# Kernel tuning notes

Measured on AMD Instinct MI355X. Metric: run time of the kernel, lower is better.

## Reference

```python
import jax, jax.numpy as jnp
import numpy as np

TOP_K = 4
EPS = 1e-6


def setup_inputs() -> dict:
    key = jax.random.key(0)
    k1, k2, k3 = jax.random.split(key, 3)
    B, Q, N, H, W = 4, 200, 32, 256, 256
    pred_masks = jax.random.normal(k1, (B, Q, H, W), dtype=jnp.float32)
    pred_logits = jax.random.normal(k2, (B, Q, 2), dtype=jnp.float32)
    gt_masks = (jax.random.uniform(k3, (B, N, H, W)) < 0.3).astype(jnp.float32)
    return {"pred_masks": pred_masks, "pred_logits": pred_logits, "gt_masks": gt_masks}


def _combined_scores(pred_masks, pred_logits, gt_masks):
    """IoU * class-score, shape [B, Q, N]."""
    pm = jax.nn.sigmoid(pred_masks)                    # [B,Q,H,W]
    cls = jax.nn.softmax(pred_logits, axis=-1)[..., 1]  # [B,Q]
    B, Q = pm.shape[:2]
    N = gt_masks.shape[1]
    pmf = pm.reshape(B, Q, -1)                         # [B,Q,D]
    tmf = gt_masks.reshape(B, N, -1)                   # [B,N,D]
    inter = jnp.einsum('bqd,bnd->bqn', pmf, tmf)
    union = pmf.sum(-1)[:, :, None] + tmf.sum(-1)[:, None, :] - inter
    iou = inter / (union + EPS)
    return iou * cls[:, :, None]


def _greedy_assign(combined):
    """Greedy per-GT top-k with dedup. combined: [Q,N] -> sel indices [N,k], -1 = dropped."""
    Q = combined.shape[0]
    k = min(TOP_K, Q)

    def step(assigned, col):
        _, idx = jax.lax.top_k(col, k)          # [k] query indices for this GT
        taken = assigned[idx]                   # already assigned -> drop
        sel = jnp.where(taken, -1, idx)
        assigned = assigned.at[idx].set(True)
        return assigned, sel

    _, sels = jax.lax.scan(step, jnp.zeros(Q, dtype=bool), combined.T)
    return sels  # [N, k]


def reference(pred_masks, pred_logits, gt_masks):
    combined = _combined_scores(pred_masks, pred_logits, gt_masks)  # [B,Q,N]
    sels = jax.vmap(_greedy_assign)(combined)                       # [B,N,k]
    B, N, k = sels.shape
    src_idx = sels
    tgt_idx = jnp.broadcast_to(jnp.arange(N, dtype=jnp.int32)[None, :, None], sels.shape)
    valid = sels >= 0
    tgt_idx = jnp.where(valid, tgt_idx, -1)
    return src_idx, tgt_idx, valid
```

## Files before the change

kernel.cpp:

```cpp
#include <hip/hip_runtime.h>
#include <math.h>
#include <stdint.h>

#define BB    4
#define QQ    200
#define NGT   32
#define DD    65536
#define TOPK  4
#define EPSF  1e-6f
#define QP    208

#define QT3   7
#define KG    64
#define NSTEP 16

typedef float  f32x4  __attribute__((ext_vector_type(4)));
typedef float  f32x16 __attribute__((ext_vector_type(16)));
typedef __bf16 bf16x8 __attribute__((ext_vector_type(8)));

__global__ __launch_bounds__(256) void k_pack(const float* __restrict__ gt,
                                              uint32_t* __restrict__ packed,
                                              float* __restrict__ zero_base) {
    int zidx = blockIdx.x * 256 + threadIdx.x;
    if (zidx < BB * NGT * QP + BB * QP) zero_base[zidx] = 0.0f;

    int blk = blockIdx.x;
    int b = blk >> 6;
    int d0 = ((blk & 63) * 256 + threadIdx.x) * 4;
    uint32_t px = 0, py = 0, pz = 0, pw = 0;
    const float* gb = gt + (size_t)b * NGT * DD + d0;
#pragma unroll
    for (int n = 0; n < NGT; ++n) {
        float4 g = *(const float4*)(gb + (size_t)n * DD);
        px |= (g.x > 0.5f ? 1u : 0u) << n;
        py |= (g.y > 0.5f ? 1u : 0u) << n;
        pz |= (g.z > 0.5f ? 1u : 0u) << n;
        pw |= (g.w > 0.5f ? 1u : 0u) << n;
    }
    *(uint4*)(packed + (size_t)b * DD + d0) = make_uint4(px, py, pz, pw);
}

__global__ __launch_bounds__(256) void k_tsum(const uint32_t* __restrict__ packed,
                                              float* __restrict__ tsum) {
    int b = blockIdx.x >> 5;
    int n = blockIdx.x & 31;
    const uint4* pp = (const uint4*)(packed + (size_t)b * DD);
    int cnt = 0;
    for (int i = threadIdx.x; i < DD / 4; i += 256) {
        uint4 w = pp[i];
        cnt += (int)((w.x >> n) & 1u) + (int)((w.y >> n) & 1u) +
               (int)((w.z >> n) & 1u) + (int)((w.w >> n) & 1u);
    }
#pragma unroll
    for (int off = 32; off; off >>= 1) cnt += __shfl_xor(cnt, off);
    __shared__ int red[4];
    if ((threadIdx.x & 63) == 0) red[threadIdx.x >> 6] = cnt;
    __syncthreads();
    if (threadIdx.x == 0)
        tsum[blockIdx.x] = (float)(red[0] + red[1] + red[2] + red[3]);
}

__global__ __launch_bounds__(256, 4) void k_mfma(const float* __restrict__ pm,
                                                 const uint32_t* __restrict__ packed,
                                                 float* __restrict__ inter,
                                                 float* __restrict__ psum) {
    int blk = blockIdx.x;
    int b   = blk / (QT3 * KG);
    int rem = blk % (QT3 * KG);
    int qt  = rem / KG;
    int kg  = rem % KG;
    int tid = threadIdx.x, lane = tid & 63, wave = tid >> 6;
    int m = lane & 31, half = lane >> 5;

    int q_glob = qt * 32 + m;
    int q_eff  = q_glob < QQ ? q_glob : QQ - 1;
    int kbase  = kg * 1024 + wave * 256;
    const float*    ap = pm + (size_t)(b * QQ + q_eff) * DD + kbase + half * 8;
    const uint32_t* bp = packed + (size_t)b * DD + kbase + half * 8;

    f32x16 c0, c1;
#pragma unroll
    for (int r = 0; r < 16; ++r) { c0[r] = 0.f; c1[r] = 0.f; }
    float ps = 0.f;
    int sh = 31 - m;

    float4 fa0 = *(const float4*)ap;
    float4 fa1 = *(const float4*)(ap + 4);
    uint4  wb0 = *(const uint4*)bp;
    uint4  wb1 = *(const uint4*)(bp + 4);

    for (int s = 0; s < NSTEP; ++s) {
        float4 a0 = fa0, a1 = fa1;
        uint4  w0 = wb0, w1 = wb1;
        if (s < NSTEP - 1) {
            const float*    apn = ap + (s + 1) * 16;
            const uint32_t* bpn = bp + (s + 1) * 16;
            fa0 = *(const float4*)apn;
            fa1 = *(const float4*)(apn + 4);
            wb0 = *(const uint4*)bpn;
            wb1 = *(const uint4*)(bpn + 4);
        }
        float xs[8] = {a0.x, a0.y, a0.z, a0.w, a1.x, a1.y, a1.z, a1.w};
        uint32_t hu[8], mu[8], lu[8];
#pragma unroll
        for (int i = 0; i < 8; ++i) {
            float x  = xs[i];
            float sg = __builtin_amdgcn_rcpf(1.0f + __expf(-x));
            ps += sg;
            uint32_t u0 = __float_as_uint(sg);
            float hi = __uint_as_float(u0 & 0xFFFF0000u);
            float r1 = sg - hi;
            uint32_t u1 = __float_as_uint(r1);
            float mi = __uint_as_float(u1 & 0xFFFF0000u);
            float r2 = r1 - mi;
            hu[i] = u0; mu[i] = u1; lu[i] = __float_as_uint(r2);
        }
        union { uint4 u; bf16x8 v; } ah, am, al, bb;
        ah.u = make_uint4((hu[0] >> 16) | (hu[1] & 0xFFFF0000u),
                          (hu[2] >> 16) | (hu[3] & 0xFFFF0000u),
                          (hu[4] >> 16) | (hu[5] & 0xFFFF0000u),
                          (hu[6] >> 16) | (hu[7] & 0xFFFF0000u));
        am.u = make_uint4((mu[0] >> 16) | (mu[1] & 0xFFFF0000u),
                          (mu[2] >> 16) | (mu[3] & 0xFFFF0000u),
                          (mu[4] >> 16) | (mu[5] & 0xFFFF0000u),
                          (mu[6] >> 16) | (mu[7] & 0xFFFF0000u));
        al.u = make_uint4((lu[0] >> 16) | (lu[1] & 0xFFFF0000u),
                          (lu[2] >> 16) | (lu[3] & 0xFFFF0000u),
                          (lu[4] >> 16) | (lu[5] & 0xFFFF0000u),
                          (lu[6] >> 16) | (lu[7] & 0xFFFF0000u));
        uint32_t wj[8] = {w0.x, w0.y, w0.z, w0.w, w1.x, w1.y, w1.z, w1.w};
        uint32_t bv[4];
#pragma unroll
        for (int d = 0; d < 4; ++d)
            bv[d] = ((uint32_t)(((int)(wj[2 * d] << sh)) >> 31) & 0x3F80u)
                  | ((uint32_t)(((int)(wj[2 * d + 1] << sh)) >> 31) & 0x3F800000u);
        bb.u = make_uint4(bv[0], bv[1], bv[2], bv[3]);

        c0 = __builtin_amdgcn_mfma_f32_32x32x16_bf16(ah.v, bb.v, c0, 0, 0, 0);
        c1 = __builtin_amdgcn_mfma_f32_32x32x16_bf16(am.v, bb.v, c1, 0, 0, 0);
        c1 = __builtin_amdgcn_mfma_f32_32x32x16_bf16(al.v, bb.v, c1, 0, 0, 0);
    }

    ps += __shfl_xor(ps, 32);
    if (lane < 32 && q_glob < QQ) atomicAdd(&psum[b * QP + q_glob], ps);

    f32x16 c;
#pragma unroll
    for (int r = 0; r < 16; ++r) c[r] = c0[r] + c1[r];

    __shared__ float cred[3 * 64 * 17];
    if (wave > 0) {
        float* dst = cred + ((wave - 1) * 64 + lane) * 17;
#pragma unroll
        for (int r = 0; r < 16; ++r) dst[r] = c[r];
    }
    __syncthreads();
    if (wave == 0) {
#pragma unroll
        for (int wv = 0; wv < 3; ++wv) {
            const float* sp = cred + (wv * 64 + lane) * 17;
#pragma unroll
            for (int r = 0; r < 16; ++r) c[r] += sp[r];
        }
#pragma unroll
        for (int r = 0; r < 16; ++r) {
            int qg = qt * 32 + (r & 3) + 8 * (r >> 2) + 4 * half;
            if (qg < QQ) atomicAdd(&inter[(b * NGT + m) * QP + qg], c[r]);
        }
    }
}

__global__ __launch_bounds__(64) void k_topk(const float* __restrict__ inter,
                                             const float* __restrict__ psum,
                                             const float* __restrict__ tsum,
                                             const float* __restrict__ logits,
                                             int* __restrict__ idx4) {
    int bn = blockIdx.x;
    int b  = bn >> 5;
    int lane = threadIdx.x;
    float tsn = tsum[bn];
    float v[4];
#pragma unroll
    for (int s = 0; s < 4; ++s) {
        int q = lane + 64 * s;
        if (q < QQ) {
            float iv = inter[(size_t)bn * QP + q];
            float un = psum[b * QP + q] + tsn - iv;
            float l0 = logits[(b * QQ + q) * 2];
            float l1 = logits[(b * QQ + q) * 2 + 1];
            float cl = 1.0f / (1.0f + expf(l0 - l1));
            v[s] = iv / (un + EPSF) * cl;
        } else {
            v[s] = -INFINITY;
        }
    }
    for (int k = 0; k < TOPK; ++k) {
        float bv = -INFINITY;
        int   bi = 0x7fffffff;
#pragma unroll
        for (int s = 0; s < 4; ++s)
            if (v[s] > bv) { bv = v[s]; bi = lane + 64 * s; }
#pragma unroll
        for (int off = 32; off; off >>= 1) {
            float ov = __shfl_xor(bv, off);
            int   oi = __shfl_xor(bi, off);
            if (ov > bv || (ov == bv && oi < bi)) { bv = ov; bi = oi; }
        }
        if (lane == (bi & 63)) v[bi >> 6] = -INFINITY;
        if (lane == 0) idx4[bn * TOPK + k] = bi;
    }
}

__global__ __launch_bounds__(64) void k_final(const int* __restrict__ idx4,
                                              int* __restrict__ out) {
    int b = blockIdx.x;
    int lane = threadIdx.x;
    int* src = out;
    int* tgt = out + BB * NGT * TOPK;
    int* val = out + 2 * BB * NGT * TOPK;
    int asg = 0;
    for (int n = 0; n < NGT; ++n) {
        int4 id = *(const int4*)&idx4[(b * NGT + n) * TOPK];
        int ids[4] = {id.x, id.y, id.z, id.w};
        int newasg = asg;
#pragma unroll
        for (int k = 0; k < TOPK; ++k) {
            int idx = ids[k];
            int owner = idx & 63, slot = idx >> 6;
            int oasg = __shfl(asg, owner);
            int taken = (oasg >> slot) & 1;
            if (lane == owner) newasg |= (1 << slot);
            if (lane == 0) {
                int o = (b * NGT + n) * TOPK + k;
                src[o] = taken ? -1 : idx;
                tgt[o] = taken ? -1 : n;
                val[o] = taken ? 0 : 1;
            }
        }
        asg = newasg;
    }
}

extern "C" void kernel_launch(void* const* d_in, const int* in_sizes, int n_in,
                              void* d_out, int out_size, void* d_ws, size_t ws_size,
                              hipStream_t stream) {
    const float* pred_masks  = (const float*)d_in[0];
    const float* pred_logits = (const float*)d_in[1];
    const float* gt_masks    = (const float*)d_in[2];

    uint8_t* ws = (uint8_t*)d_ws;
    uint32_t* packed = (uint32_t*)ws;
    float* tsum  = (float*)(ws + (size_t)BB * DD * 4);
    float* inter = tsum + BB * NGT;
    float* psum  = inter + BB * NGT * QP;
    int*   idx4  = (int*)(psum + BB * QP);

    k_pack <<<BB * (DD / 1024), 256, 0, stream>>>(gt_masks, packed, inter);
    k_tsum <<<BB * NGT,         256, 0, stream>>>(packed, tsum);
    k_mfma <<<BB * QT3 * KG,    256, 0, stream>>>(pred_masks, packed, inter, psum);
    k_topk <<<BB * NGT,          64, 0, stream>>>(inter, psum, tsum, pred_logits, idx4);
    k_final<<<BB,                64, 0, stream>>>(idx4, (int*)d_out);
}
```

Before: 382.9 us.

## Restructure MFMA kernel into 16x16x32 tiles with double-buffered LDS staging

```diff
diff --git a/kernel.cpp b/kernel.cpp
--- a/kernel.cpp
+++ b/kernel.cpp
@@ -10,13 +10,20 @@
 #define EPSF  1e-6f
 #define QP    208
 
-#define QT3   7
-#define KG    64
-#define NSTEP 16
+#define QT16  13
+#define KG    16
+#define KSPAN (DD / KG)
+#define BK    256
+#define NCH   (KSPAN / BK)
+#define RS    260
 
 typedef float  f32x4  __attribute__((ext_vector_type(4)));
-typedef float  f32x16 __attribute__((ext_vector_type(16)));
 typedef __bf16 bf16x8 __attribute__((ext_vector_type(8)));
+
+#define GLOAD_LDS16(gp, lp)                                                       \
+    __builtin_amdgcn_global_load_lds(                                             \
+        (const __attribute__((address_space(1))) void*)(gp),                      \
+        (__attribute__((address_space(3))) void*)(lp), 16, 0, 0)
 
 __global__ __launch_bounds__(256) void k_pack(const float* __restrict__ gt,
                                               uint32_t* __restrict__ packed,
@@ -65,107 +72,135 @@
                                                  float* __restrict__ inter,
                                                  float* __restrict__ psum) {
     int blk = blockIdx.x;
-    int b   = blk / (QT3 * KG);
-    int rem = blk % (QT3 * KG);
+    int b   = blk / (QT16 * KG);
+    int rem = blk % (QT16 * KG);
     int qt  = rem / KG;
     int kg  = rem % KG;
     int tid = threadIdx.x, lane = tid & 63, wave = tid >> 6;
-    int m = lane & 31, half = lane >> 5;
-
-    int q_glob = qt * 32 + m;
-    int q_eff  = q_glob < QQ ? q_glob : QQ - 1;
-    int kbase  = kg * 1024 + wave * 256;
-    const float*    ap = pm + (size_t)(b * QQ + q_eff) * DD + kbase + half * 8;
-    const uint32_t* bp = packed + (size_t)b * DD + kbase + half * 8;
-
-    f32x16 c0, c1;
-#pragma unroll
-    for (int r = 0; r < 16; ++r) { c0[r] = 0.f; c1[r] = 0.f; }
+    int m = lane & 15, quad = lane >> 4;
+
+    __shared__ float    sA[2][16][RS];
+    __shared__ uint32_t sB[2][BK];
+
+    const size_t kbase = (size_t)kg * KSPAN;
+    const float*    pmb = pm + (size_t)b * QQ * DD + kbase;
+    const uint32_t* pkb = packed + (size_t)b * DD + kbase;
+
+    auto stage = [&](int c, int bf) {
+#pragma unroll
+        for (int i = 0; i < 4; ++i) {
+            int row = wave * 4 + i;
+            int qg  = qt * 16 + row;
+            int qe  = qg < QQ ? qg : QQ - 1;
+            const float* gp = pmb + (size_t)qe * DD + c * BK + lane * 4;
+            GLOAD_LDS16(gp, &sA[bf][row][0]);
+        }
+        if (wave == 0) {
+            const uint32_t* gp = pkb + c * BK + lane * 4;
+            GLOAD_LDS16(gp, &sB[bf][0]);
+        }
+    };
+
+    f32x4 cH0 = {0.f,0.f,0.f,0.f}, cL0 = {0.f,0.f,0.f,0.f};
+    f32x4 cH1 = {0.f,0.f,0.f,0.f}, cL1 = {0.f,0.f,0.f,0.f};
     float ps = 0.f;
-    int sh = 31 - m;
-
-    float4 fa0 = *(const float4*)ap;
-    float4 fa1 = *(const float4*)(ap + 4);
-    uint4  wb0 = *(const uint4*)bp;
-    uint4  wb1 = *(const uint4*)(bp + 4);
-
-    for (int s = 0; s < NSTEP; ++s) {
-        float4 a0 = fa0, a1 = fa1;
-        uint4  w0 = wb0, w1 = wb1;
-        if (s < NSTEP - 1) {
-            const float*    apn = ap + (s + 1) * 16;
-            const uint32_t* bpn = bp + (s + 1) * 16;
-            fa0 = *(const float4*)apn;
-            fa1 = *(const float4*)(apn + 4);
-            wb0 = *(const uint4*)bpn;
-            wb1 = *(const uint4*)(bpn + 4);
-        }
-        float xs[8] = {a0.x, a0.y, a0.z, a0.w, a1.x, a1.y, a1.z, a1.w};
-        uint32_t hu[8], mu[8], lu[8];
-#pragma unroll
-        for (int i = 0; i < 8; ++i) {
-            float x  = xs[i];
-            float sg = __builtin_amdgcn_rcpf(1.0f + __expf(-x));
-            ps += sg;
-            uint32_t u0 = __float_as_uint(sg);
-            float hi = __uint_as_float(u0 & 0xFFFF0000u);
-            float r1 = sg - hi;
-            uint32_t u1 = __float_as_uint(r1);
-            float mi = __uint_as_float(u1 & 0xFFFF0000u);
-            float r2 = r1 - mi;
-            hu[i] = u0; mu[i] = u1; lu[i] = __float_as_uint(r2);
-        }
-        union { uint4 u; bf16x8 v; } ah, am, al, bb;
-        ah.u = make_uint4((hu[0] >> 16) | (hu[1] & 0xFFFF0000u),
-                          (hu[2] >> 16) | (hu[3] & 0xFFFF0000u),
-                          (hu[4] >> 16) | (hu[5] & 0xFFFF0000u),
-                          (hu[6] >> 16) | (hu[7] & 0xFFFF0000u));
-        am.u = make_uint4((mu[0] >> 16) | (mu[1] & 0xFFFF0000u),
-                          (mu[2] >> 16) | (mu[3] & 0xFFFF0000u),
-                          (mu[4] >> 16) | (mu[5] & 0xFFFF0000u),
-                          (mu[6] >> 16) | (mu[7] & 0xFFFF0000u));
-        al.u = make_uint4((lu[0] >> 16) | (lu[1] & 0xFFFF0000u),
-                          (lu[2] >> 16) | (lu[3] & 0xFFFF0000u),
-                          (lu[4] >> 16) | (lu[5] & 0xFFFF0000u),
-                          (lu[6] >> 16) | (lu[7] & 0xFFFF0000u));
-        uint32_t wj[8] = {w0.x, w0.y, w0.z, w0.w, w1.x, w1.y, w1.z, w1.w};
-        uint32_t bv[4];
-#pragma unroll
-        for (int d = 0; d < 4; ++d)
-            bv[d] = ((uint32_t)(((int)(wj[2 * d] << sh)) >> 31) & 0x3F80u)
-                  | ((uint32_t)(((int)(wj[2 * d + 1] << sh)) >> 31) & 0x3F800000u);
-        bb.u = make_uint4(bv[0], bv[1], bv[2], bv[3]);
-
-        c0 = __builtin_amdgcn_mfma_f32_32x32x16_bf16(ah.v, bb.v, c0, 0, 0, 0);
-        c1 = __builtin_amdgcn_mfma_f32_32x32x16_bf16(am.v, bb.v, c1, 0, 0, 0);
-        c1 = __builtin_amdgcn_mfma_f32_32x32x16_bf16(al.v, bb.v, c1, 0, 0, 0);
-    }
-
+
+    stage(0, 0);
+    for (int c = 0; c < NCH; ++c) {
+        __builtin_amdgcn_s_waitcnt(0);
+        __syncthreads();
+        if (c + 1 < NCH) stage(c + 1, (c + 1) & 1);
+        int bf = c & 1;
+#pragma unroll
+        for (int st = 0; st < 2; ++st) {
+            int k0 = (wave * 2 + st) * 32 + quad * 8;
+            float4 a0 = *(const float4*)&sA[bf][m][k0];
+            float4 a1 = *(const float4*)&sA[bf][m][k0 + 4];
+            uint4  w0 = *(const uint4*)&sB[bf][k0];
+            uint4  w1 = *(const uint4*)&sB[bf][k0 + 4];
+
+            float xs[8] = {a0.x, a0.y, a0.z, a0.w, a1.x, a1.y, a1.z, a1.w};
+            uint32_t hu[8], mu[8], lu[8];
+#pragma unroll
+            for (int i = 0; i < 8; ++i) {
+                float x  = xs[i];
+                float sg = __builtin_amdgcn_rcpf(1.0f + __expf(-x));
+                ps += sg;
+                uint32_t u0 = __float_as_uint(sg);
+                float hi = __uint_as_float(u0 & 0xFFFF0000u);
+                float r1 = sg - hi;
+                uint32_t u1 = __float_as_uint(r1);
+                float mi = __uint_as_float(u1 & 0xFFFF0000u);
+                float r2 = r1 - mi;
+                hu[i] = u0; mu[i] = u1; lu[i] = __float_as_uint(r2);
+            }
+            union { uint4 u; bf16x8 v; } ah, am, al;
+            ah.u = make_uint4((hu[0] >> 16) | (hu[1] & 0xFFFF0000u),
+                              (hu[2] >> 16) | (hu[3] & 0xFFFF0000u),
+                              (hu[4] >> 16) | (hu[5] & 0xFFFF0000u),
+                              (hu[6] >> 16) | (hu[7] & 0xFFFF0000u));
+            am.u = make_uint4((mu[0] >> 16) | (mu[1] & 0xFFFF0000u),
+                              (mu[2] >> 16) | (mu[3] & 0xFFFF0000u),
+                              (mu[4] >> 16) | (mu[5] & 0xFFFF0000u),
+                              (mu[6] >> 16) | (mu[7] & 0xFFFF0000u));
+            al.u = make_uint4((lu[0] >> 16) | (lu[1] & 0xFFFF0000u),
+                              (lu[2] >> 16) | (lu[3] & 0xFFFF0000u),
+                              (lu[4] >> 16) | (lu[5] & 0xFFFF0000u),
+                              (lu[6] >> 16) | (lu[7] & 0xFFFF0000u));
+
+            uint32_t wj[8] = {w0.x, w0.y, w0.z, w0.w, w1.x, w1.y, w1.z, w1.w};
+            union { ushort u[8]; bf16x8 v; } b0, b1;
+#pragma unroll
+            for (int j = 0; j < 8; ++j) {
+                b0.u[j] = (ushort)((((int)(wj[j] << (31 - m))) >> 31) & 0x3F80);
+                b1.u[j] = (ushort)((((int)(wj[j] << (15 - m))) >> 31) & 0x3F80);
+            }
+
+            cH0 = __builtin_amdgcn_mfma_f32_16x16x32_bf16(ah.v, b0.v, cH0, 0, 0, 0);
+            cL0 = __builtin_amdgcn_mfma_f32_16x16x32_bf16(am.v, b0.v, cL0, 0, 0, 0);
+            cL0 = __builtin_amdgcn_mfma_f32_16x16x32_bf16(al.v, b0.v, cL0, 0, 0, 0);
+            cH1 = __builtin_amdgcn_mfma_f32_16x16x32_bf16(ah.v, b1.v, cH1, 0, 0, 0);
+            cL1 = __builtin_amdgcn_mfma_f32_16x16x32_bf16(am.v, b1.v, cL1, 0, 0, 0);
+            cL1 = __builtin_amdgcn_mfma_f32_16x16x32_bf16(al.v, b1.v, cL1, 0, 0, 0);
+        }
+    }
+
+    ps += __shfl_xor(ps, 16);
     ps += __shfl_xor(ps, 32);
-    if (lane < 32 && q_glob < QQ) atomicAdd(&psum[b * QP + q_glob], ps);
-
-    f32x16 c;
-#pragma unroll
-    for (int r = 0; r < 16; ++r) c[r] = c0[r] + c1[r];
-
-    __shared__ float cred[3 * 64 * 17];
+    if (lane < 16) {
+        int qg = qt * 16 + m;
+        if (qg < QQ) atomicAdd(&psum[b * QP + qg], ps);
+    }
+
+    float c8[8];
+#pragma unroll
+    for (int r = 0; r < 4; ++r) {
+        c8[r]     = cH0[r] + cL0[r];
+        c8[4 + r] = cH1[r] + cL1[r];
+    }
+    __builtin_amdgcn_s_waitcnt(0);
+    __syncthreads();
+    float* cred = (float*)sA;
     if (wave > 0) {
-        float* dst = cred + ((wave - 1) * 64 + lane) * 17;
-#pragma unroll
-        for (int r = 0; r < 16; ++r) dst[r] = c[r];
+        float* dst = cred + ((wave - 1) * 64 + lane) * 9;
+#pragma unroll
+        for (int r = 0; r < 8; ++r) dst[r] = c8[r];
     }
     __syncthreads();
     if (wave == 0) {
 #pragma unroll
         for (int wv = 0; wv < 3; ++wv) {
-            const float* sp = cred + (wv * 64 + lane) * 17;
-#pragma unroll
-            for (int r = 0; r < 16; ++r) c[r] += sp[r];
-        }
-#pragma unroll
-        for (int r = 0; r < 16; ++r) {
-            int qg = qt * 32 + (r & 3) + 8 * (r >> 2) + 4 * half;
-            if (qg < QQ) atomicAdd(&inter[(b * NGT + m) * QP + qg], c[r]);
+            const float* sp = cred + (wv * 64 + lane) * 9;
+#pragma unroll
+            for (int r = 0; r < 8; ++r) c8[r] += sp[r];
+        }
+#pragma unroll
+        for (int r = 0; r < 4; ++r) {
+            int qg = qt * 16 + quad * 4 + r;
+            if (qg < QQ) {
+                atomicAdd(&inter[(b * NGT + m) * QP + qg],      c8[r]);
+                atomicAdd(&inter[(b * NGT + 16 + m) * QP + qg], c8[4 + r]);
+            }
         }
     }
 }
@@ -257,7 +292,7 @@
 
     k_pack <<<BB * (DD / 1024), 256, 0, stream>>>(gt_masks, packed, inter);
     k_tsum <<<BB * NGT,         256, 0, stream>>>(packed, tsum);
-    k_mfma <<<BB * QT3 * KG,    256, 0, stream>>>(pred_masks, packed, inter, psum);
+    k_mfma <<<BB * QT16 * KG,   256, 0, stream>>>(pred_masks, packed, inter, psum);
     k_topk <<<BB * NGT,          64, 0, stream>>>(inter, psum, tsum, pred_logits, idx4);
     k_final<<<BB,                64, 0, stream>>>(idx4, (int*)d_out);
 }
```

After: 354.1 us. 1.08x faster.
